# Performance work log

Hardware: AMD Instinct MI355X
Metric: run time of the kernel (lower is better)

## Reference

```python
import jax, jax.numpy as jnp
import numpy as np

B, S, D, H = 64, 32, 1024, 1024


def setup_inputs() -> dict:
    key = jax.random.key(0)
    ks = jax.random.split(key, 12)
    sd = 1.0 / np.sqrt(D)
    sh = 1.0 / np.sqrt(H)
    return {
        "local_descs_t": jax.random.normal(ks[0], (B, S, D), jnp.float32),
        "local_descs_rot": jax.random.normal(ks[1], (B, S, D), jnp.float32),
        "scene_w": jax.random.normal(ks[2], (2 * D,), jnp.float32) * sd,
        "scene_b": jax.random.normal(ks[3], (1,), jnp.float32),
        "Wt1": jax.random.normal(ks[4], (S, D, H), jnp.float32) * sd,
        "bt1": jax.random.normal(ks[5], (S, H), jnp.float32) * 0.01,
        "Wt2": jax.random.normal(ks[6], (S, H, 3), jnp.float32) * sh,
        "bt2": jax.random.normal(ks[7], (S, 3), jnp.float32) * 0.01,
        "Wr1": jax.random.normal(ks[8], (S, D, H), jnp.float32) * sd,
        "br1": jax.random.normal(ks[9], (S, H), jnp.float32) * 0.01,
        "Wr2": jax.random.normal(ks[10], (S, H, 4), jnp.float32) * sh,
        "br2": jax.random.normal(ks[11], (S, 4), jnp.float32) * 0.01,
    }


def _pose_head(g, idx, W1, b1, W2, b2):
    # g: [B, D]; gather per-sample expert weights and run 2-layer MLP (GELU, exact erf as in F.gelu)
    h = jax.nn.gelu(jnp.einsum("bd,bdh->bh", g, W1[idx]) + b1[idx], approximate=False)
    return jnp.einsum("bh,bho->bo", h, W2[idx]) + b2[idx]


def reference(local_descs_t, local_descs_rot, scene_w, scene_b,
              Wt1, bt1, Wt2, bt2, Wr1, br1, Wr2, br2):
    # scene classification: Linear(2D -> 1) over concat descriptors, log-softmax over scenes
    logits = jnp.einsum("bsd,d->bs",
                        jnp.concatenate([local_descs_t, local_descs_rot], axis=2),
                        scene_w) + scene_b  # [B, S]
    scene_log_distr = jax.nn.log_softmax(logits, axis=1)
    idx = jnp.argmax(scene_log_distr, axis=1)  # top-1 scene per sample, [B]
    # select the chosen scene's descriptor (equivalent to one-hot mask * descs, summed over scenes)
    global_desc_t = jnp.take_along_axis(local_descs_t, idx[:, None, None], axis=1)[:, 0]    # [B, D]
    global_desc_rot = jnp.take_along_axis(local_descs_rot, idx[:, None, None], axis=1)[:, 0]
    # per-sample expert head dispatch (use_prior=False)
    x_t = _pose_head(global_desc_t, idx, Wt1, bt1, Wt2, bt2)      # [B, 3]
    x_rot = _pose_head(global_desc_rot, idx, Wr1, br1, Wr2, br2)  # [B, 4]
    expected_pose = jnp.concatenate([x_t, x_rot], axis=1)          # [B, 7]
    return expected_pose, scene_log_distr
```

## Files before the change

kernel.cpp:

```cpp
#include <hip/hip_runtime.h>
#include <math.h>

#define BB 64
#define SS 32
#define DD 1024
#define HH 1024
#define PMAX 8

__device__ __forceinline__ float gelu_exact(float x) {
    return 0.5f * x * (1.0f + erff(x * 0.7071067811865476f));
}

#define WS_LOGITS 256
#define WS_LIST   8448
#define WS_COUNT  16640
#define WS_PART   32768

__global__ __launch_bounds__(256) void logits_kernel(
    const float* __restrict__ descs_t, const float* __restrict__ descs_rot,
    const float* __restrict__ scene_w, float* __restrict__ logits)
{
    const int s = blockIdx.x, b = blockIdx.y;
    const int tid = threadIdx.x, lane = tid & 63, wave = tid >> 6;

    const float4* t4 = (const float4*)(descs_t  + ((size_t)b * SS + s) * DD);
    const float4* r4 = (const float4*)(descs_rot + ((size_t)b * SS + s) * DD);
    const float4* w4t = (const float4*)(scene_w);
    const float4* w4r = (const float4*)(scene_w + DD);

    float4 a = t4[tid], w = w4t[tid];
    float acc = a.x*w.x + a.y*w.y + a.z*w.z + a.w*w.w;
    float4 a2 = r4[tid], w2 = w4r[tid];
    acc += a2.x*w2.x + a2.y*w2.y + a2.z*w2.z + a2.w*w2.w;

    #pragma unroll
    for (int off = 32; off >= 1; off >>= 1) acc += __shfl_xor(acc, off, 64);

    __shared__ float red[4];
    if (lane == 0) red[wave] = acc;
    __syncthreads();
    if (tid == 0) logits[b * SS + s] = red[0] + red[1] + red[2] + red[3];
}

__global__ __launch_bounds__(64) void finalize_scene_kernel(
    const float* __restrict__ scene_b, float* __restrict__ logits,
    int* __restrict__ idx_ws, int* __restrict__ list, int* __restrict__ count,
    float* __restrict__ out)
{
    const int b = threadIdx.x;
    const float bias = scene_b[0];
    float lg[SS];
    float m = -1e30f; int am = 0;
    #pragma unroll
    for (int s = 0; s < SS; ++s) {
        lg[s] = logits[b * SS + s] + bias;
        if (lg[s] > m) { m = lg[s]; am = s; }
    }
    float sum = 0.f;
    #pragma unroll
    for (int s = 0; s < SS; ++s) sum += expf(lg[s] - m);
    const float lse = m + logf(sum);
    #pragma unroll
    for (int s = 0; s < SS; ++s) out[BB * 7 + b * SS + s] = lg[s] - lse;
    idx_ws[b] = am;

    for (int s = 0; s < SS; ++s) {
        unsigned long long mk = __ballot(am == s);
        if (am == s) {
            int rank = __popcll(mk & ((1ull << b) - 1ull));
            list[s * BB + rank] = b;
        }
        if (b == 0) count[s] = (int)__popcll(mk);
    }
}

template<int DSPL>
__global__ __launch_bounds__(256) void layer1_kernel(
    const float* __restrict__ descs_t, const float* __restrict__ descs_rot,
    const float* __restrict__ Wt1, const float* __restrict__ Wr1,
    const int* __restrict__ list, const int* __restrict__ count,
    float* __restrict__ part)
{
    constexpr int DS = DD / DSPL;
    const int dsp  = blockIdx.x;
    const int s    = blockIdx.y;
    const int head = blockIdx.z;
    const int tid  = threadIdx.x;

    const int cnt = count[s];
    if (cnt == 0) return;

    __shared__ int   sh_list[BB];
    __shared__ float sh_g[PMAX][DS];
    if (tid < BB) sh_list[tid] = list[s * BB + tid];

    const float* descs = head ? descs_rot : descs_t;
    const float* W = (head ? Wr1 : Wt1) + (size_t)s * DD * HH;
    const int j  = tid * 4;
    const int d0 = dsp * DS;

    for (int p0 = 0; p0 < cnt; p0 += PMAX) {
        const int nb = min(PMAX, cnt - p0);
        __syncthreads();
        for (int t = tid; t < PMAX * (DS / 4); t += 256) {
            const int p = t / (DS / 4);
            const int c = t % (DS / 4);
            float4 v = make_float4(0.f, 0.f, 0.f, 0.f);
            if (p < nb) {
                const int b = sh_list[p0 + p];
                v = ((const float4*)(descs + ((size_t)b * SS + s) * DD + d0))[c];
            }
            ((float4*)sh_g[p])[c] = v;
        }
        __syncthreads();

        float4 acc[PMAX];
        #pragma unroll
        for (int p = 0; p < PMAX; ++p) acc[p] = make_float4(0.f, 0.f, 0.f, 0.f);

        const float* Wd = W + (size_t)d0 * HH + j;
        #pragma unroll 2
        for (int d8 = 0; d8 < DS / 8; ++d8) {
            float4 w[8];
            #pragma unroll
            for (int r = 0; r < 8; ++r)
                w[r] = *(const float4*)(Wd + (size_t)(d8 * 8 + r) * HH);
            #pragma unroll
            for (int h4 = 0; h4 < 2; ++h4) {
                #pragma unroll
                for (int p = 0; p < PMAX; ++p) {
                    float4 g = ((const float4*)sh_g[p])[d8 * 2 + h4];
                    acc[p].x += g.x * w[h4*4+0].x; acc[p].y += g.x * w[h4*4+0].y;
                    acc[p].z += g.x * w[h4*4+0].z; acc[p].w += g.x * w[h4*4+0].w;
                    acc[p].x += g.y * w[h4*4+1].x; acc[p].y += g.y * w[h4*4+1].y;
                    acc[p].z += g.y * w[h4*4+1].z; acc[p].w += g.y * w[h4*4+1].w;
                    acc[p].x += g.z * w[h4*4+2].x; acc[p].y += g.z * w[h4*4+2].y;
                    acc[p].z += g.z * w[h4*4+2].z; acc[p].w += g.z * w[h4*4+2].w;
                    acc[p].x += g.w * w[h4*4+3].x; acc[p].y += g.w * w[h4*4+3].y;
                    acc[p].z += g.w * w[h4*4+3].z; acc[p].w += g.w * w[h4*4+3].w;
                }
            }
        }

        #pragma unroll
        for (int p = 0; p < PMAX; ++p) {
            if (p < nb) {
                const int b = sh_list[p0 + p];
                float* dst = part + (((size_t)(head * BB + b) * DSPL + dsp) * HH) + j;
                *(float4*)dst = acc[p];
            }
        }
    }
}

template<int DSPL>
__global__ __launch_bounds__(256) void head_out_kernel(
    const float* __restrict__ bt1, const float* __restrict__ Wt2, const float* __restrict__ bt2,
    const float* __restrict__ br1, const float* __restrict__ Wr2, const float* __restrict__ br2,
    const int* __restrict__ idx_ws, const float* __restrict__ part,
    float* __restrict__ out)
{
    const int b   = blockIdx.x;
    const int tid = threadIdx.x;
    const int s   = idx_ws[b];

    __shared__ float sh_h[2][HH];
    __shared__ float sh_red[7][4];

    #pragma unroll
    for (int head = 0; head < 2; ++head) {
        const float* b1 = (head ? br1 : bt1) + (size_t)s * HH;
        const float* p0 = part + ((size_t)(head * BB + b) * DSPL) * HH;
        const int j = tid * 4;
        float4 a = *(const float4*)(p0 + j);
        #pragma unroll
        for (int dsp = 1; dsp < DSPL; ++dsp) {
            float4 q = *(const float4*)(p0 + (size_t)dsp * HH + j);
            a.x += q.x; a.y += q.y; a.z += q.z; a.w += q.w;
        }
        float4 bb = *(const float4*)(b1 + j);
        sh_h[head][j + 0] = gelu_exact(a.x + bb.x);
        sh_h[head][j + 1] = gelu_exact(a.y + bb.y);
        sh_h[head][j + 2] = gelu_exact(a.z + bb.z);
        sh_h[head][j + 3] = gelu_exact(a.w + bb.w);
    }
    __syncthreads();

    const float* wt2 = Wt2 + (size_t)s * HH * 3;
    const float* wr2 = Wr2 + (size_t)s * HH * 4;
    float pa[7] = {0.f, 0.f, 0.f, 0.f, 0.f, 0.f, 0.f};
    for (int j = tid; j < HH; j += 256) {
        float ht = sh_h[0][j];
        float hr = sh_h[1][j];
        pa[0] += ht * wt2[j * 3 + 0];
        pa[1] += ht * wt2[j * 3 + 1];
        pa[2] += ht * wt2[j * 3 + 2];
        pa[3] += hr * wr2[j * 4 + 0];
        pa[4] += hr * wr2[j * 4 + 1];
        pa[5] += hr * wr2[j * 4 + 2];
        pa[6] += hr * wr2[j * 4 + 3];
    }
    const int lane = tid & 63, wave = tid >> 6;
    #pragma unroll
    for (int o = 0; o < 7; ++o) {
        float v = pa[o];
        #pragma unroll
        for (int off = 32; off >= 1; off >>= 1) v += __shfl_xor(v, off, 64);
        if (lane == 0) sh_red[o][wave] = v;
    }
    __syncthreads();
    if (tid < 7) {
        float v = sh_red[tid][0] + sh_red[tid][1] + sh_red[tid][2] + sh_red[tid][3];
        float bias = (tid < 3) ? bt2[(size_t)s * 3 + tid] : br2[(size_t)s * 4 + (tid - 3)];
        out[b * 7 + tid] = v + bias;
    }
}

template<int DSPL>
static void launch_pipeline(const float* descs_t, const float* descs_rot,
                            const float* Wt1, const float* Wr1,
                            const float* bt1, const float* Wt2, const float* bt2,
                            const float* br1, const float* Wr2, const float* br2,
                            int* idx_ws, int* list, int* count, float* part,
                            float* out, hipStream_t stream) {
    layer1_kernel<DSPL><<<dim3(DSPL, SS, 2), dim3(256), 0, stream>>>(
        descs_t, descs_rot, Wt1, Wr1, list, count, part);
    head_out_kernel<DSPL><<<dim3(BB), dim3(256), 0, stream>>>(
        bt1, Wt2, bt2, br1, Wr2, br2, idx_ws, part, out);
}

extern "C" void kernel_launch(void* const* d_in, const int* in_sizes, int n_in,
                              void* d_out, int out_size, void* d_ws, size_t ws_size,
                              hipStream_t stream) {
    const float* descs_t   = (const float*)d_in[0];
    const float* descs_rot = (const float*)d_in[1];
    const float* scene_w   = (const float*)d_in[2];
    const float* scene_b   = (const float*)d_in[3];
    const float* Wt1 = (const float*)d_in[4];
    const float* bt1 = (const float*)d_in[5];
    const float* Wt2 = (const float*)d_in[6];
    const float* bt2 = (const float*)d_in[7];
    const float* Wr1 = (const float*)d_in[8];
    const float* br1 = (const float*)d_in[9];
    const float* Wr2 = (const float*)d_in[10];
    const float* br2 = (const float*)d_in[11];
    float* out = (float*)d_out;

    int*   idx_ws = (int*)d_ws;
    float* logits = (float*)((char*)d_ws + WS_LOGITS);
    int*   list   = (int*)((char*)d_ws + WS_LIST);
    int*   count  = (int*)((char*)d_ws + WS_COUNT);
    float* part   = (float*)((char*)d_ws + WS_PART);

    logits_kernel<<<dim3(SS, BB), dim3(256), 0, stream>>>(
        descs_t, descs_rot, scene_w, logits);
    finalize_scene_kernel<<<dim3(1), dim3(64), 0, stream>>>(
        scene_b, logits, idx_ws, list, count, out);

    const size_t need16 = (size_t)WS_PART + (size_t)2 * BB * 16 * HH * sizeof(float);
    const size_t need8  = (size_t)WS_PART + (size_t)2 * BB * 8  * HH * sizeof(float);
    if (ws_size >= need16) {
        launch_pipeline<16>(descs_t, descs_rot, Wt1, Wr1, bt1, Wt2, bt2, br1, Wr2, br2,
                            idx_ws, list, count, part, out, stream);
    } else if (ws_size >= need8) {
        launch_pipeline<8>(descs_t, descs_rot, Wt1, Wr1, bt1, Wt2, bt2, br1, Wr2, br2,
                            idx_ws, list, count, part, out, stream);
    } else {
        launch_pipeline<4>(descs_t, descs_rot, Wt1, Wr1, bt1, Wt2, bt2, br1, Wr2, br2,
                            idx_ws, list, count, part, out, stream);
    }
}
```

Measured before the change: 63.55 us.

## Replace scene-grouped layer1 with per-sample blocks indexed by chosen scene

```diff
diff --git a/kernel.cpp b/kernel.cpp
--- a/kernel.cpp
+++ b/kernel.cpp
@@ -5,15 +5,12 @@
 #define SS 32
 #define DD 1024
 #define HH 1024
-#define PMAX 8
 
 __device__ __forceinline__ float gelu_exact(float x) {
     return 0.5f * x * (1.0f + erff(x * 0.7071067811865476f));
 }
 
 #define WS_LOGITS 256
-#define WS_LIST   8448
-#define WS_COUNT  16640
 #define WS_PART   32768
 
 __global__ __launch_bounds__(256) void logits_kernel(
@@ -44,8 +41,7 @@
 
 __global__ __launch_bounds__(64) void finalize_scene_kernel(
     const float* __restrict__ scene_b, float* __restrict__ logits,
-    int* __restrict__ idx_ws, int* __restrict__ list, int* __restrict__ count,
-    float* __restrict__ out)
+    int* __restrict__ idx_ws, float* __restrict__ out)
 {
     const int b = threadIdx.x;
     const float bias = scene_b[0];
@@ -63,94 +59,49 @@
     #pragma unroll
     for (int s = 0; s < SS; ++s) out[BB * 7 + b * SS + s] = lg[s] - lse;
     idx_ws[b] = am;
-
-    for (int s = 0; s < SS; ++s) {
-        unsigned long long mk = __ballot(am == s);
-        if (am == s) {
-            int rank = __popcll(mk & ((1ull << b) - 1ull));
-            list[s * BB + rank] = b;
-        }
-        if (b == 0) count[s] = (int)__popcll(mk);
-    }
 }
 
 template<int DSPL>
 __global__ __launch_bounds__(256) void layer1_kernel(
     const float* __restrict__ descs_t, const float* __restrict__ descs_rot,
     const float* __restrict__ Wt1, const float* __restrict__ Wr1,
-    const int* __restrict__ list, const int* __restrict__ count,
-    float* __restrict__ part)
+    const int* __restrict__ idx_ws, float* __restrict__ part)
 {
     constexpr int DS = DD / DSPL;
     const int dsp  = blockIdx.x;
-    const int s    = blockIdx.y;
+    const int b    = blockIdx.y;
     const int head = blockIdx.z;
     const int tid  = threadIdx.x;
-
-    const int cnt = count[s];
-    if (cnt == 0) return;
-
-    __shared__ int   sh_list[BB];
-    __shared__ float sh_g[PMAX][DS];
-    if (tid < BB) sh_list[tid] = list[s * BB + tid];
-
+    const int s    = idx_ws[b];
+
+    __shared__ float sh_g[DS];
     const float* descs = head ? descs_rot : descs_t;
-    const float* W = (head ? Wr1 : Wt1) + (size_t)s * DD * HH;
-    const int j  = tid * 4;
-    const int d0 = dsp * DS;
-
-    for (int p0 = 0; p0 < cnt; p0 += PMAX) {
-        const int nb = min(PMAX, cnt - p0);
-        __syncthreads();
-        for (int t = tid; t < PMAX * (DS / 4); t += 256) {
-            const int p = t / (DS / 4);
-            const int c = t % (DS / 4);
-            float4 v = make_float4(0.f, 0.f, 0.f, 0.f);
-            if (p < nb) {
-                const int b = sh_list[p0 + p];
-                v = ((const float4*)(descs + ((size_t)b * SS + s) * DD + d0))[c];
-            }
-            ((float4*)sh_g[p])[c] = v;
+    if (tid < DS / 4) {
+        ((float4*)sh_g)[tid] =
+            ((const float4*)(descs + ((size_t)b * SS + s) * DD + dsp * DS))[tid];
+    }
+    __syncthreads();
+
+    const float* W = (head ? Wr1 : Wt1)
+                   + (size_t)s * DD * HH + (size_t)dsp * DS * HH + tid * 4;
+    float4 acc = make_float4(0.f, 0.f, 0.f, 0.f);
+
+    #pragma unroll
+    for (int d0 = 0; d0 < DS; d0 += 16) {
+        float4 w[16];
+        #pragma unroll
+        for (int r = 0; r < 16; ++r)
+            w[r] = *(const float4*)(W + (size_t)(d0 + r) * HH);
+        #pragma unroll
+        for (int r = 0; r < 16; ++r) {
+            const float g = sh_g[d0 + r];
+            acc.x += g * w[r].x; acc.y += g * w[r].y;
+            acc.z += g * w[r].z; acc.w += g * w[r].w;
         }
-        __syncthreads();
-
-        float4 acc[PMAX];
-        #pragma unroll
-        for (int p = 0; p < PMAX; ++p) acc[p] = make_float4(0.f, 0.f, 0.f, 0.f);
-
-        const float* Wd = W + (size_t)d0 * HH + j;
-        #pragma unroll 2
-        for (int d8 = 0; d8 < DS / 8; ++d8) {
-            float4 w[8];
-            #pragma unroll
-            for (int r = 0; r < 8; ++r)
-                w[r] = *(const float4*)(Wd + (size_t)(d8 * 8 + r) * HH);
-            #pragma unroll
-            for (int h4 = 0; h4 < 2; ++h4) {
-                #pragma unroll
-                for (int p = 0; p < PMAX; ++p) {
-                    float4 g = ((const float4*)sh_g[p])[d8 * 2 + h4];
-                    acc[p].x += g.x * w[h4*4+0].x; acc[p].y += g.x * w[h4*4+0].y;
-                    acc[p].z += g.x * w[h4*4+0].z; acc[p].w += g.x * w[h4*4+0].w;
-                    acc[p].x += g.y * w[h4*4+1].x; acc[p].y += g.y * w[h4*4+1].y;
-                    acc[p].z += g.y * w[h4*4+1].z; acc[p].w += g.y * w[h4*4+1].w;
-                    acc[p].x += g.z * w[h4*4+2].x; acc[p].y += g.z * w[h4*4+2].y;
-                    acc[p].z += g.z * w[h4*4+2].z; acc[p].w += g.z * w[h4*4+2].w;
-                    acc[p].x += g.w * w[h4*4+3].x; acc[p].y += g.w * w[h4*4+3].y;
-                    acc[p].z += g.w * w[h4*4+3].z; acc[p].w += g.w * w[h4*4+3].w;
-                }
-            }
-        }
-
-        #pragma unroll
-        for (int p = 0; p < PMAX; ++p) {
-            if (p < nb) {
-                const int b = sh_list[p0 + p];
-                float* dst = part + (((size_t)(head * BB + b) * DSPL + dsp) * HH) + j;
-                *(float4*)dst = acc[p];
-            }
-        }
-    }
+    }
+
+    float* dst = part + (((size_t)(head * BB + b) * DSPL + dsp) * HH) + tid * 4;
+    *(float4*)dst = acc;
 }
 
 template<int DSPL>
@@ -221,10 +172,10 @@
                             const float* Wt1, const float* Wr1,
                             const float* bt1, const float* Wt2, const float* bt2,
                             const float* br1, const float* Wr2, const float* br2,
-                            int* idx_ws, int* list, int* count, float* part,
+                            int* idx_ws, float* part,
                             float* out, hipStream_t stream) {
-    layer1_kernel<DSPL><<<dim3(DSPL, SS, 2), dim3(256), 0, stream>>>(
-        descs_t, descs_rot, Wt1, Wr1, list, count, part);
+    layer1_kernel<DSPL><<<dim3(DSPL, BB, 2), dim3(256), 0, stream>>>(
+        descs_t, descs_rot, Wt1, Wr1, idx_ws, part);
     head_out_kernel<DSPL><<<dim3(BB), dim3(256), 0, stream>>>(
         bt1, Wt2, bt2, br1, Wr2, br2, idx_ws, part, out);
 }
@@ -248,25 +199,23 @@
 
     int*   idx_ws = (int*)d_ws;
     float* logits = (float*)((char*)d_ws + WS_LOGITS);
-    int*   list   = (int*)((char*)d_ws + WS_LIST);
-    int*   count  = (int*)((char*)d_ws + WS_COUNT);
     float* part   = (float*)((char*)d_ws + WS_PART);
 
     logits_kernel<<<dim3(SS, BB), dim3(256), 0, stream>>>(
         descs_t, descs_rot, scene_w, logits);
     finalize_scene_kernel<<<dim3(1), dim3(64), 0, stream>>>(
-        scene_b, logits, idx_ws, list, count, out);
+        scene_b, logits, idx_ws, out);
 
     const size_t need16 = (size_t)WS_PART + (size_t)2 * BB * 16 * HH * sizeof(float);
     const size_t need8  = (size_t)WS_PART + (size_t)2 * BB * 8  * HH * sizeof(float);
     if (ws_size >= need16) {
         launch_pipeline<16>(descs_t, descs_rot, Wt1, Wr1, bt1, Wt2, bt2, br1, Wr2, br2,
-                            idx_ws, list, count, part, out, stream);
+                            idx_ws, part, out, stream);
     } else if (ws_size >= need8) {
         launch_pipeline<8>(descs_t, descs_rot, Wt1, Wr1, bt1, Wt2, bt2, br1, Wr2, br2,
-                            idx_ws, list, count, part, out, stream);
+                            idx_ws, part, out, stream);
     } else {
         launch_pipeline<4>(descs_t, descs_rot, Wt1, Wr1, bt1, Wt2, bt2, br1, Wr2, br2,
-                            idx_ws, list, count, part, out, stream);
-    }
-}
+                            idx_ws, part, out, stream);
+    }
+}
```

Measured after the change: 74.09 us. 16.6% more time.
